# Kernel tuning notes

Hardware: AMD Instinct MI355X
Metric: run time of the kernel (lower is better)

## Reference

```python
import jax, jax.numpy as jnp
import numpy as np
from jax import lax

B = 4096
SRC = 50   # source_seq_len (encoder runs SRC-1 steps)
TGT = 25   # target_seq_len
R = 1024   # rnn_size
H = 67     # HUMAN_SIZE
I = 82     # input_size = 67 + 15 one-hot actions


def gru_cell(x, h, Wi, Wh, bi, bh):
    # torch.nn.GRUCell semantics; gate order (r, z, n); Wi:[3R,in], Wh:[3R,R]
    gi = x @ Wi.T + bi
    gh = h @ Wh.T + bh
    ir, iz, inn = jnp.split(gi, 3, axis=1)
    hr, hz, hn = jnp.split(gh, 3, axis=1)
    r = jax.nn.sigmoid(ir + hr)
    z = jax.nn.sigmoid(iz + hz)
    n = jnp.tanh(inn + r * hn)
    return (1.0 - z) * n + z * h


def setup_inputs() -> dict:
    key = jax.random.key(0)
    ks = jax.random.split(key, 12)
    s = 0.05
    return {
        "encoder_inputs": jax.random.normal(ks[0], (B, SRC - 1, I), jnp.float32),
        "decoder_inputs": jax.random.normal(ks[1], (B, TGT, I), jnp.float32),
        "Wi1": jax.random.normal(ks[2], (3 * R, I), jnp.float32) * s,
        "Wh1": jax.random.normal(ks[3], (3 * R, R), jnp.float32) * s,
        "bi1": jax.random.normal(ks[4], (3 * R,), jnp.float32) * s,
        "bh1": jax.random.normal(ks[5], (3 * R,), jnp.float32) * s,
        "Wi2": jax.random.normal(ks[6], (3 * R, R), jnp.float32) * s,
        "Wh2": jax.random.normal(ks[7], (3 * R, R), jnp.float32) * s,
        "bi2": jax.random.normal(ks[8], (3 * R,), jnp.float32) * s,
        "bh2": jax.random.normal(ks[9], (3 * R,), jnp.float32) * s,
        "Wfc": jax.random.normal(ks[10], (H, 2 * R), jnp.float32) * s,
        "bfc": jax.random.normal(ks[11], (H,), jnp.float32) * s,
        "use_cuda": 0,
    }


def reference(encoder_inputs, decoder_inputs, Wi1, Wh1, bi1, bh1,
              Wi2, Wh2, bi2, bh2, Wfc, bfc, use_cuda):
    # dropout=0.0 / eval mode -> dropout is identity (faithful to module defaults)
    bsz = encoder_inputs.shape[0]
    enc = jnp.transpose(encoder_inputs, (1, 0, 2))  # [SRC-1, B, I]
    dec = jnp.transpose(decoder_inputs, (1, 0, 2))  # [TGT,   B, I]

    s1 = jnp.zeros((bsz, R), encoder_inputs.dtype)
    s2 = jnp.zeros((bsz, R), encoder_inputs.dtype)

    def enc_step(carry, x):
        s1, s2 = carry
        s1 = gru_cell(x, s1, Wi1, Wh1, bi1, bh1)
        s2 = gru_cell(s1, s2, Wi2, Wh2, bi2, bh2)
        return (s1, s2), None

    (s1, s2), _ = lax.scan(enc_step, (s1, s2), enc)

    # decoder feeds back previous output (loop_function = identity on prev)
    prev0 = dec[0][:, :H]

    def dec_step(carry, dec_t):
        s1, s2, prev = carry
        inp = lax.stop_gradient(jnp.concatenate([prev, dec_t[:, H:]], axis=1))  # .detach()
        s1 = gru_cell(inp, s1, Wi1, Wh1, bi1, bh1)
        s2 = gru_cell(s1, s2, Wi2, Wh2, bi2, bh2)
        state_out = jnp.concatenate([s1, s2], axis=1)          # [B, 2R]
        out = inp[:, :H] + state_out @ Wfc.T + bfc             # residual velocities
        return (s1, s2, out), out

    _, outputs = lax.scan(dec_step, (s1, s2, prev0), dec)      # [TGT, B, H]
    return jnp.transpose(outputs, (1, 0, 2))                   # [B, TGT, H]
```

## Files before the change

### kernel.cpp

```cpp
#include <hip/hip_runtime.h>
#include <hip/hip_bf16.h>
#include <math.h>

#define B_        4096
#define ENC_STEPS 49
#define TGT_      25
#define R_        1024
#define H_        67
#define I_        82
#define IP_       96
#define IP2_      192
#define NG_       3072
#define FCN_      128
#define K2_       2048

typedef unsigned short u16;
typedef __attribute__((ext_vector_type(8))) short bf16x8_t;
typedef __attribute__((ext_vector_type(4))) float f32x4_t;

__device__ __forceinline__ float bf2f(u16 h) {
    union { unsigned int u; float f; } v; v.u = ((unsigned int)h) << 16; return v.f;
}
__device__ __forceinline__ u16 f2bf(float f) {
    union { unsigned int u; float f; } v; v.f = f;
    unsigned int u = v.u;
    u += 0x7fffu + ((u >> 16) & 1u);
    return (u16)(u >> 16);
}
__device__ __forceinline__ float sigmf(float x) { return 1.f / (1.f + __expf(-x)); }
__device__ __forceinline__ float tanhfast(float x) { return 1.f - 2.f / (__expf(2.f * x) + 1.f); }

__device__ __forceinline__ void g2l16(const u16* g, u16* l) {
    __builtin_amdgcn_global_load_lds(
        (const __attribute__((address_space(1))) unsigned int*)(const void*)g,
        (__attribute__((address_space(3))) unsigned int*)(void*)l,
        16, 0, 0);
}

__global__ void cast_bf16_kernel(const float* __restrict__ s, u16* __restrict__ d, int n) {
    int i = blockIdx.x * 256 + threadIdx.x;
    if (i < n) d[i] = f2bf(s[i]);
}
__global__ void pad_wi1_dup_kernel(const float* __restrict__ s, u16* __restrict__ d) {
    int i = blockIdx.x * 256 + threadIdx.x;
    if (i >= NG_ * IP2_) return;
    int r = i / IP2_, c = i % IP2_;
    int cc = (c < IP_) ? c : c - IP_;
    d[i] = (cc < I_) ? f2bf(s[r * I_ + cc]) : (u16)0;
}
__global__ void pad_wfc_kernel(const float* __restrict__ s, u16* __restrict__ d) {
    int i = blockIdx.x * 256 + threadIdx.x;
    if (i >= FCN_ * K2_) return;
    int r = i / K2_, c = i % K2_;
    d[i] = (r < H_) ? f2bf(s[r * K2_ + c]) : (u16)0;
}

__global__ void pad_all_x_kernel(const float* __restrict__ enc, u16* __restrict__ xall) {
    int i = blockIdx.x * 256 + threadIdx.x;
    if (i >= B_ * ENC_STEPS * IP_) return;
    int c = i % IP_;
    int t = (i / IP_) % ENC_STEPS;
    int b = i / (IP_ * ENC_STEPS);
    float v = (c < I_) ? enc[((size_t)b * ENC_STEPS + t) * I_ + c] : 0.f;
    u16 hi = f2bf(v);
    u16 lo = f2bf(v - bf2f(hi));
    size_t base = ((size_t)t * B_ + b) * IP2_;
    xall[base + c]       = hi;
    xall[base + IP_ + c] = lo;
}

__global__ void build_inp_kernel(const float* __restrict__ prev, int pstride,
                                 const float* __restrict__ dec, int t,
                                 u16* __restrict__ xpad) {
    int i = blockIdx.x * 256 + threadIdx.x;
    if (i >= B_ * IP_) return;
    int b = i / IP_, c = i % IP_;
    float v = 0.f;
    if (c < H_)      v = prev[(size_t)b * pstride + c];
    else if (c < I_) v = dec[((size_t)b * TGT_ + t) * I_ + c];
    u16 hi = f2bf(v);
    u16 lo = f2bf(v - bf2f(hi));
    xpad[(size_t)b * IP2_ + c]       = hi;
    xpad[(size_t)b * IP2_ + IP_ + c] = lo;
}

template<int KX>
__global__ __launch_bounds__(256, 2) void gru_step_kernel(
    const u16* __restrict__ Ax, int ldax,
    const u16* __restrict__ Wx,
    const u16* __restrict__ Ah, int ldah,
    const u16* __restrict__ Wh,
    const float* __restrict__ bi, const float* __restrict__ bh,
    float* __restrict__ hf,
    u16* __restrict__ hout)
{
    __shared__ __align__(16) u16 As[3][128 * 32];
    __shared__ __align__(16) u16 Ws[3][3 * 64 * 32];

    const int tid  = threadIdx.x;
    const int lane = tid & 63, wave = tid >> 6;
    const int wm = wave >> 1, wn = wave & 1;
    const int mbase = blockIdx.y * 128;
    const int nbase = blockIdx.x * 64;
    const int lr = lane & 15;
    const int sw = (((lane >> 4) ^ ((lr >> 1) & 3)) * 8);

    constexpr int NX = KX / 32;
    constexpr int NT = NX + R_ / 32;

    f32x4_t acc_r[4][2], acc_z[4][2], acc_xn[4][2], acc_hn[4][2];
#pragma unroll
    for (int i = 0; i < 4; i++)
#pragma unroll
        for (int j = 0; j < 2; j++) {
            acc_r[i][j]  = (f32x4_t){0,0,0,0};
            acc_z[i][j]  = (f32x4_t){0,0,0,0};
            acc_xn[i][j] = (f32x4_t){0,0,0,0};
            acc_hn[i][j] = (f32x4_t){0,0,0,0};
        }

    auto stage = [&](int s, int b) {
        const u16* A; int lda; const u16* W; int ldw; int k0;
        if (s < NX) { A = Ax; lda = ldax; W = Wx; ldw = KX; k0 = s * 32; }
        else        { A = Ah; lda = ldah; W = Wh; ldw = R_;  k0 = (s - NX) * 32; }
#pragma unroll
        for (int p = 0; p < 2; p++) {
            int g = tid + p * 256;
            int row = g >> 2;
            int ch  = (g & 3) ^ ((row >> 1) & 3);
            g2l16(A + (size_t)(mbase + row) * lda + k0 + ch * 8, As[b] + g * 8);
        }
#pragma unroll
        for (int p = 0; p < 3; p++) {
            int q = tid + p * 256;
            int row = q >> 2;
            int gate = q >> 8, rg = (q >> 2) & 63;
            int cw = (q & 3) ^ ((row >> 1) & 3);
            g2l16(W + ((size_t)gate * R_ + nbase + rg) * ldw + k0 + cw * 8, Ws[b] + q * 8);
        }
    };

    auto compute = [&](int s, int b) {
        bf16x8_t a_f[4], w_r[2], w_z[2], w_n[2];
#pragma unroll
        for (int i = 0; i < 4; i++)
            a_f[i] = *(const bf16x8_t*)(As[b] + (wm * 64 + i * 16 + lr) * 32 + sw);
#pragma unroll
        for (int j = 0; j < 2; j++) {
            int c = wn * 32 + j * 16 + lr;
            w_r[j] = *(const bf16x8_t*)(Ws[b] + c * 32 + sw);
            w_z[j] = *(const bf16x8_t*)(Ws[b] + (64 + c) * 32 + sw);
            w_n[j] = *(const bf16x8_t*)(Ws[b] + (128 + c) * 32 + sw);
        }
        __builtin_amdgcn_s_setprio(1);
#pragma unroll
        for (int i = 0; i < 4; i++)
#pragma unroll
            for (int j = 0; j < 2; j++) {
                acc_r[i][j] = __builtin_amdgcn_mfma_f32_16x16x32_bf16(a_f[i], w_r[j], acc_r[i][j], 0, 0, 0);
                acc_z[i][j] = __builtin_amdgcn_mfma_f32_16x16x32_bf16(a_f[i], w_z[j], acc_z[i][j], 0, 0, 0);
            }
        if (s < NX) {
#pragma unroll
            for (int i = 0; i < 4; i++)
#pragma unroll
                for (int j = 0; j < 2; j++)
                    acc_xn[i][j] = __builtin_amdgcn_mfma_f32_16x16x32_bf16(a_f[i], w_n[j], acc_xn[i][j], 0, 0, 0);
        } else {
#pragma unroll
            for (int i = 0; i < 4; i++)
#pragma unroll
                for (int j = 0; j < 2; j++)
                    acc_hn[i][j] = __builtin_amdgcn_mfma_f32_16x16x32_bf16(a_f[i], w_n[j], acc_hn[i][j], 0, 0, 0);
        }
        __builtin_amdgcn_s_setprio(0);
    };

    stage(0, 0);
    stage(1, 1);
    int b = 0;
    for (int s = 0; s < NT; ++s) {
        if (s + 2 < NT) {
            asm volatile("s_waitcnt vmcnt(5)" ::: "memory");
            __builtin_amdgcn_s_barrier();
            __builtin_amdgcn_sched_barrier(0);
            int b2 = b + 2; if (b2 >= 3) b2 -= 3;
            stage(s + 2, b2);
        } else {
            asm volatile("s_waitcnt vmcnt(0)" ::: "memory");
            __builtin_amdgcn_s_barrier();
            __builtin_amdgcn_sched_barrier(0);
        }
        compute(s, b);
        if (++b == 3) b = 0;
    }

    const int rr2 = (lane >> 4) * 4;
#pragma unroll
    for (int j = 0; j < 2; j++) {
        const int col = nbase + wn * 32 + j * 16 + lr;
        const float b_ir = bi[col],          b_hr = bh[col];
        const float b_iz = bi[R_ + col],     b_hz = bh[R_ + col];
        const float b_in = bi[2 * R_ + col], b_hn = bh[2 * R_ + col];
#pragma unroll
        for (int i = 0; i < 4; i++) {
#pragma unroll
            for (int r = 0; r < 4; r++) {
                const int row = mbase + wm * 64 + i * 16 + rr2 + r;
                const float hold = hf[(size_t)row * R_ + col];
                const float rv = sigmf(acc_r[i][j][r] + b_ir + b_hr);
                const float zv = sigmf(acc_z[i][j][r] + b_iz + b_hz);
                const float nv = tanhfast(acc_xn[i][j][r] + b_in + rv * (acc_hn[i][j][r] + b_hn));
                const float hn = (1.f - zv) * nv + zv * hold;
                hf[(size_t)row * R_ + col] = hn;
                hout[(size_t)row * K2_ + col] = f2bf(hn);
            }
        }
    }
}

__global__ __launch_bounds__(256) void fc_part_kernel(
    const u16* __restrict__ A, const u16* __restrict__ W, float* __restrict__ part) {
    __shared__ __align__(16) u16 As[64 * 32];
    __shared__ __align__(16) u16 Bs[128 * 32];
    const int tid  = threadIdx.x;
    const int lane = tid & 63, wave = tid >> 6;
    const int wm = wave >> 1, wn = wave & 1;
    const int mbase = blockIdx.y * 64;
    const int kbase = blockIdx.x * 512;
    const int lr = lane & 15;
    const int sw = (((lane >> 4) ^ ((lr >> 1) & 3)) * 8);

    f32x4_t acc[2][4];
#pragma unroll
    for (int i = 0; i < 2; i++)
#pragma unroll
        for (int j = 0; j < 4; j++) acc[i][j] = (f32x4_t){0, 0, 0, 0};

    for (int k0 = 0; k0 < 512; k0 += 32) {
        __syncthreads();
        {
            int g = tid;
            int row = g >> 2;
            int ch  = (g & 3) ^ ((row >> 1) & 3);
            g2l16(A + (size_t)(mbase + row) * K2_ + kbase + k0 + ch * 8, As + g * 8);
        }
#pragma unroll
        for (int p = 0; p < 2; p++) {
            int q = tid + p * 256;
            int row = q >> 2;
            int cw  = (q & 3) ^ ((row >> 1) & 3);
            g2l16(W + (size_t)row * K2_ + kbase + k0 + cw * 8, Bs + q * 8);
        }
        __syncthreads();
        bf16x8_t a_f[2], b_f[4];
#pragma unroll
        for (int i = 0; i < 2; i++)
            a_f[i] = *(const bf16x8_t*)(As + (wm * 32 + i * 16 + lr) * 32 + sw);
#pragma unroll
        for (int j = 0; j < 4; j++)
            b_f[j] = *(const bf16x8_t*)(Bs + (wn * 64 + j * 16 + lr) * 32 + sw);
#pragma unroll
        for (int i = 0; i < 2; i++)
#pragma unroll
            for (int j = 0; j < 4; j++)
                acc[i][j] = __builtin_amdgcn_mfma_f32_16x16x32_bf16(a_f[i], b_f[j], acc[i][j], 0, 0, 0);
    }
    const int rr2 = (lane >> 4) * 4;
#pragma unroll
    for (int i = 0; i < 2; i++)
#pragma unroll
        for (int r = 0; r < 4; r++) {
            int row = mbase + wm * 32 + i * 16 + rr2 + r;
#pragma unroll
            for (int j = 0; j < 4; j++) {
                int col = wn * 64 + j * 16 + lr;
                part[((size_t)blockIdx.x * B_ + row) * FCN_ + col] = acc[i][j][r];
            }
        }
}

__global__ void fc_finish_kernel(const float* __restrict__ part, const float* __restrict__ prev,
                                 int pstride, const float* __restrict__ bfc,
                                 float* __restrict__ out, int t,
                                 const float* __restrict__ dec, u16* __restrict__ xpad,
                                 int write_x) {
    int i = blockIdx.x * 256 + threadIdx.x;
    if (i >= B_ * IP_) return;
    int b = i / IP_, c = i % IP_;
    float v = 0.f;
    if (c < H_) {
        size_t idx = (size_t)b * FCN_ + c;
        const size_t S = (size_t)B_ * FCN_;
        float s = (part[idx] + part[S + idx]) + (part[2 * S + idx] + part[3 * S + idx]);
        v = prev[(size_t)b * pstride + c] + s + bfc[c];
        out[((size_t)b * TGT_ + t) * H_ + c] = v;
    } else if (c < I_ && write_x) {
        v = dec[((size_t)b * TGT_ + (t + 1)) * I_ + c];
    }
    if (write_x) {
        u16 hi = f2bf(v);
        u16 lo = f2bf(v - bf2f(hi));
        xpad[(size_t)b * IP2_ + c]       = hi;
        xpad[(size_t)b * IP2_ + IP_ + c] = lo;
    }
}

extern "C" void kernel_launch(void* const* d_in, const int* in_sizes, int n_in,
                              void* d_out, int out_size, void* d_ws, size_t ws_size,
                              hipStream_t stream) {
    (void)in_sizes; (void)n_in; (void)out_size; (void)ws_size;
    const float* enc = (const float*)d_in[0];
    const float* dec = (const float*)d_in[1];
    const float* Wi1 = (const float*)d_in[2];
    const float* Wh1 = (const float*)d_in[3];
    const float* bi1 = (const float*)d_in[4];
    const float* bh1 = (const float*)d_in[5];
    const float* Wi2 = (const float*)d_in[6];
    const float* Wh2 = (const float*)d_in[7];
    const float* bi2 = (const float*)d_in[8];
    const float* bh2 = (const float*)d_in[9];
    const float* Wfc = (const float*)d_in[10];
    const float* bfc = (const float*)d_in[11];
    float* out = (float*)d_out;

    char* ws = (char*)d_ws;
    size_t off = 0;
    auto alloc = [&](size_t bytes) -> char* {
        char* p = ws + off;
        off += (bytes + 255) & ~(size_t)255;
        return p;
    };
    u16* Wh1b  = (u16*)alloc((size_t)NG_ * R_ * 2);
    u16* Wi2b  = (u16*)alloc((size_t)NG_ * R_ * 2);
    u16* Wh2b  = (u16*)alloc((size_t)NG_ * R_ * 2);
    u16* Wi1pb = (u16*)alloc((size_t)NG_ * IP2_ * 2);
    u16* Wfcb  = (u16*)alloc((size_t)FCN_ * K2_ * 2);
    u16* sbuf0 = (u16*)alloc((size_t)B_ * K2_ * 2);
    float* s1f = (float*)alloc((size_t)B_ * R_ * 4);
    float* s2f = (float*)alloc((size_t)B_ * R_ * 4);
    u16* sbuf1 = (u16*)alloc((size_t)B_ * K2_ * 2);
    u16* xall  = (u16*)alloc((size_t)ENC_STEPS * B_ * IP2_ * 2);
    u16* xpad2 = (u16*)alloc((size_t)B_ * IP2_ * 2);
    float* cfcp = (float*)alloc((size_t)4 * B_ * FCN_ * 4);
    u16* sbuf[2] = { sbuf0, sbuf1 };

    hipMemsetAsync(sbuf0, 0,
                   (size_t)B_ * K2_ * 2 + 2 * (size_t)B_ * R_ * 4, stream);

    cast_bf16_kernel<<<(NG_ * R_ + 255) / 256, 256, 0, stream>>>(Wh1, Wh1b, NG_ * R_);
    cast_bf16_kernel<<<(NG_ * R_ + 255) / 256, 256, 0, stream>>>(Wi2, Wi2b, NG_ * R_);
    cast_bf16_kernel<<<(NG_ * R_ + 255) / 256, 256, 0, stream>>>(Wh2, Wh2b, NG_ * R_);
    pad_wi1_dup_kernel<<<(NG_ * IP2_ + 255) / 256, 256, 0, stream>>>(Wi1, Wi1pb);
    pad_wfc_kernel<<<(FCN_ * K2_ + 255) / 256, 256, 0, stream>>>(Wfc, Wfcb);
    pad_all_x_kernel<<<(B_ * ENC_STEPS * IP_ + 255) / 256, 256, 0, stream>>>(enc, xall);

    dim3 gru_grid(R_ / 64, B_ / 128, 1);
    dim3 fc_grid(4, B_ / 64, 1);
    const int binp_blocks = (B_ * IP_ + 255) / 256;
    const int fcf_blocks  = (B_ * IP_ + 255) / 256;

    int phase = 0;

    for (int t = 0; t < ENC_STEPS; t++) {
        u16* cur = sbuf[phase];
        u16* nxt = sbuf[phase ^ 1];
        gru_step_kernel<IP2_><<<gru_grid, 256, 0, stream>>>(
            xall + (size_t)t * B_ * IP2_, IP2_, Wi1pb,
            cur, K2_, Wh1b, bi1, bh1, s1f, nxt);
        gru_step_kernel<R_><<<gru_grid, 256, 0, stream>>>(
            nxt, K2_, Wi2b,
            cur + R_, K2_, Wh2b, bi2, bh2, s2f, nxt + R_);
        phase ^= 1;
    }

    build_inp_kernel<<<binp_blocks, 256, 0, stream>>>(dec, TGT_ * I_, dec, 0, xpad2);
    for (int t = 0; t < TGT_; t++) {
        const float* prev;
        int pstride;
        if (t == 0) { prev = dec;                 pstride = TGT_ * I_; }
        else        { prev = out + (t - 1) * H_;  pstride = TGT_ * H_; }
        u16* cur = sbuf[phase];
        u16* nxt = sbuf[phase ^ 1];
        gru_step_kernel<IP2_><<<gru_grid, 256, 0, stream>>>(
            xpad2, IP2_, Wi1pb,
            cur, K2_, Wh1b, bi1, bh1, s1f, nxt);
        gru_step_kernel<R_><<<gru_grid, 256, 0, stream>>>(
            nxt, K2_, Wi2b,
            cur + R_, K2_, Wh2b, bi2, bh2, s2f, nxt + R_);
        fc_part_kernel<<<fc_grid, 256, 0, stream>>>(nxt, Wfcb, cfcp);
        fc_finish_kernel<<<fcf_blocks, 256, 0, stream>>>(
            cfcp, prev, pstride, bfc, out, t, dec, xpad2, (t < TGT_ - 1) ? 1 : 0);
        phase ^= 1;
    }
}
```

Baseline: 8.817 ms.

## Replace triple-buffered K=32 pipeline with single-buffer K=64 tiles and syncthreads

```diff
diff --git a/kernel.cpp b/kernel.cpp
--- a/kernel.cpp
+++ b/kernel.cpp
@@ -94,8 +94,8 @@
     float* __restrict__ hf,
     u16* __restrict__ hout)
 {
-    __shared__ __align__(16) u16 As[3][128 * 32];
-    __shared__ __align__(16) u16 Ws[3][3 * 64 * 32];
+    __shared__ __align__(16) u16 As[128 * 64];
+    __shared__ __align__(16) u16 Ws[3 * 64 * 64];
 
     const int tid  = threadIdx.x;
     const int lane = tid & 63, wave = tid >> 6;
@@ -103,10 +103,10 @@
     const int mbase = blockIdx.y * 128;
     const int nbase = blockIdx.x * 64;
     const int lr = lane & 15;
-    const int sw = (((lane >> 4) ^ ((lr >> 1) & 3)) * 8);
-
-    constexpr int NX = KX / 32;
-    constexpr int NT = NX + R_ / 32;
+    const int swkey = lr & 7;
+
+    constexpr int NX = KX / 64;
+    constexpr int NH = R_ / 64;
 
     f32x4_t acc_r[4][2], acc_z[4][2], acc_xn[4][2], acc_hn[4][2];
 #pragma unroll
@@ -119,80 +119,75 @@
             acc_hn[i][j] = (f32x4_t){0,0,0,0};
         }
 
-    auto stage = [&](int s, int b) {
-        const u16* A; int lda; const u16* W; int ldw; int k0;
-        if (s < NX) { A = Ax; lda = ldax; W = Wx; ldw = KX; k0 = s * 32; }
-        else        { A = Ah; lda = ldah; W = Wh; ldw = R_;  k0 = (s - NX) * 32; }
-#pragma unroll
-        for (int p = 0; p < 2; p++) {
+    auto stage = [&](const u16* A, int lda, const u16* W, int ldw, int k0) {
+#pragma unroll
+        for (int p = 0; p < 4; p++) {
             int g = tid + p * 256;
-            int row = g >> 2;
-            int ch  = (g & 3) ^ ((row >> 1) & 3);
-            g2l16(A + (size_t)(mbase + row) * lda + k0 + ch * 8, As[b] + g * 8);
-        }
-#pragma unroll
-        for (int p = 0; p < 3; p++) {
+            int row = g >> 3;
+            int ch  = (g & 7) ^ (row & 7);
+            g2l16(A + (size_t)(mbase + row) * lda + k0 + ch * 8, As + g * 8);
+        }
+#pragma unroll
+        for (int p = 0; p < 6; p++) {
             int q = tid + p * 256;
-            int row = q >> 2;
-            int gate = q >> 8, rg = (q >> 2) & 63;
-            int cw = (q & 3) ^ ((row >> 1) & 3);
-            g2l16(W + ((size_t)gate * R_ + nbase + rg) * ldw + k0 + cw * 8, Ws[b] + q * 8);
+            int row = q >> 3;
+            int gate = row >> 6, rg = row & 63;
+            int cw = (q & 7) ^ (row & 7);
+            g2l16(W + ((size_t)gate * R_ + nbase + rg) * ldw + k0 + cw * 8, Ws + q * 8);
         }
     };
 
-    auto compute = [&](int s, int b) {
-        bf16x8_t a_f[4], w_r[2], w_z[2], w_n[2];
-#pragma unroll
-        for (int i = 0; i < 4; i++)
-            a_f[i] = *(const bf16x8_t*)(As[b] + (wm * 64 + i * 16 + lr) * 32 + sw);
-#pragma unroll
-        for (int j = 0; j < 2; j++) {
-            int c = wn * 32 + j * 16 + lr;
-            w_r[j] = *(const bf16x8_t*)(Ws[b] + c * 32 + sw);
-            w_z[j] = *(const bf16x8_t*)(Ws[b] + (64 + c) * 32 + sw);
-            w_n[j] = *(const bf16x8_t*)(Ws[b] + (128 + c) * 32 + sw);
-        }
-        __builtin_amdgcn_s_setprio(1);
-#pragma unroll
-        for (int i = 0; i < 4; i++)
+    auto compute = [&](bool xpass) {
+#pragma unroll
+        for (int kk = 0; kk < 2; kk++) {
+            const int pos = ((kk * 4 + (lane >> 4)) ^ swkey) * 8;
+            bf16x8_t a_f[4], w_r[2], w_z[2], w_n[2];
+#pragma unroll
+            for (int i = 0; i < 4; i++)
+                a_f[i] = *(const bf16x8_t*)(As + (wm * 64 + i * 16 + lr) * 64 + pos);
 #pragma unroll
             for (int j = 0; j < 2; j++) {
-                acc_r[i][j] = __builtin_amdgcn_mfma_f32_16x16x32_bf16(a_f[i], w_r[j], acc_r[i][j], 0, 0, 0);
-                acc_z[i][j] = __builtin_amdgcn_mfma_f32_16x16x32_bf16(a_f[i], w_z[j], acc_z[i][j], 0, 0, 0);
+                int c = wn * 32 + j * 16 + lr;
+                w_r[j] = *(const bf16x8_t*)(Ws + c * 64 + pos);
+                w_z[j] = *(const bf16x8_t*)(Ws + (64 + c) * 64 + pos);
+                w_n[j] = *(const bf16x8_t*)(Ws + (128 + c) * 64 + pos);
             }
-        if (s < NX) {
+            __builtin_amdgcn_s_setprio(1);
 #pragma unroll
             for (int i = 0; i < 4; i++)
 #pragma unroll
-                for (int j = 0; j < 2; j++)
-                    acc_xn[i][j] = __builtin_amdgcn_mfma_f32_16x16x32_bf16(a_f[i], w_n[j], acc_xn[i][j], 0, 0, 0);
-        } else {
-#pragma unroll
-            for (int i = 0; i < 4; i++)
-#pragma unroll
-                for (int j = 0; j < 2; j++)
-                    acc_hn[i][j] = __builtin_amdgcn_mfma_f32_16x16x32_bf16(a_f[i], w_n[j], acc_hn[i][j], 0, 0, 0);
-        }
-        __builtin_amdgcn_s_setprio(0);
+                for (int j = 0; j < 2; j++) {
+                    acc_r[i][j] = __builtin_amdgcn_mfma_f32_16x16x32_bf16(a_f[i], w_r[j], acc_r[i][j], 0, 0, 0);
+                    acc_z[i][j] = __builtin_amdgcn_mfma_f32_16x16x32_bf16(a_f[i], w_z[j], acc_z[i][j], 0, 0, 0);
+                }
+            if (xpass) {
+#pragma unroll
+                for (int i = 0; i < 4; i++)
+#pragma unroll
+                    for (int j = 0; j < 2; j++)
+                        acc_xn[i][j] = __builtin_amdgcn_mfma_f32_16x16x32_bf16(a_f[i], w_n[j], acc_xn[i][j], 0, 0, 0);
+            } else {
+#pragma unroll
+                for (int i = 0; i < 4; i++)
+#pragma unroll
+                    for (int j = 0; j < 2; j++)
+                        acc_hn[i][j] = __builtin_amdgcn_mfma_f32_16x16x32_bf16(a_f[i], w_n[j], acc_hn[i][j], 0, 0, 0);
+            }
+            __builtin_amdgcn_s_setprio(0);
+        }
     };
 
-    stage(0, 0);
-    stage(1, 1);
-    int b = 0;
-    for (int s = 0; s < NT; ++s) {
-        if (s + 2 < NT) {
-            asm volatile("s_waitcnt vmcnt(5)" ::: "memory");
-            __builtin_amdgcn_s_barrier();
-            __builtin_amdgcn_sched_barrier(0);
-            int b2 = b + 2; if (b2 >= 3) b2 -= 3;
-            stage(s + 2, b2);
-        } else {
-            asm volatile("s_waitcnt vmcnt(0)" ::: "memory");
-            __builtin_amdgcn_s_barrier();
-            __builtin_amdgcn_sched_barrier(0);
-        }
-        compute(s, b);
-        if (++b == 3) b = 0;
+    for (int s = 0; s < NX; s++) {
+        __syncthreads();
+        stage(Ax, ldax, Wx, KX, s * 64);
+        __syncthreads();
+        compute(true);
+    }
+    for (int s = 0; s < NH; s++) {
+        __syncthreads();
+        stage(Ah, ldah, Wh, R_, s * 64);
+        __syncthreads();
+        compute(false);
     }
 
     const int rr2 = (lane >> 4) * 4;
```

After: 7.432 ms. 1.19x faster.
